# Performance work log

Measured on AMD Instinct MI355X. Metric: run time of the kernel, lower is better.

## Reference

```python
import jax, jax.numpy as jnp
from jax import lax
import numpy as np


def setup_inputs() -> dict:
    B, P, L, H, T = 4, 160, 128, 768, 9
    rng = np.random.default_rng(0)
    sent_length = rng.integers(L // 2, L + 1, size=B)
    sent_length[0] = L  # ensure max length equals L (pad_packed total_length)
    p2w = np.zeros((B, L, P), dtype=bool)
    for bi in range(B):
        pos = 1  # skip [CLS]
        for w in range(int(sent_length[bi])):
            n = 1 + int(rng.random() < 0.2)  # avg ~1.2 pieces per word
            if pos >= P - 1:
                break
            end = min(pos + n, P - 1)
            p2w[bi, w, pos:end] = True
            pos = end
    masks = np.arange(L)[None, :] < sent_length[:, None]
    labels = rng.integers(0, T, size=(B, L))
    key = jax.random.key(0)
    k1, k2, k3, k4, k5 = jax.random.split(key, 5)
    return {
        "bert_embs": jax.random.normal(k1, (B, P, H), jnp.float32),
        "pieces2word": jnp.asarray(p2w),
        "masks": jnp.asarray(masks),
        "labels": jnp.asarray(labels, jnp.int32),
        "sent_length": jnp.asarray(sent_length, jnp.int32),
        "W": jax.random.normal(k2, (H, T), jnp.float32) * 0.02,
        "b": jnp.zeros((T,), jnp.float32),
        "start_transitions": jax.random.uniform(k3, (T,), jnp.float32, -0.1, 0.1),
        "end_transitions": jax.random.uniform(k4, (T,), jnp.float32, -0.1, 0.1),
        "transitions": jax.random.uniform(k5, (T, T), jnp.float32, -0.1, 0.1),
    }


def crf_log_likelihood(emissions, tags, mask, start_t, end_t, trans):
    # torchcrf CRF forward (batch_first): log p(tags | emissions)
    B, L, T = emissions.shape
    maskf = mask.astype(emissions.dtype)
    barange = jnp.arange(B)
    # numerator: score of the gold tag sequence
    first_tags = tags[:, 0]
    num0 = start_t[first_tags] + emissions[barange, 0, first_tags]

    def num_step(s, inp):
        em_t, tp, tc, m = inp  # em_t: (B,T)
        return s + (trans[tp, tc] + em_t[barange, tc]) * m, None

    num, _ = lax.scan(
        num_step, num0,
        (emissions[:, 1:].transpose(1, 0, 2), tags[:, :-1].T, tags[:, 1:].T, maskf[:, 1:].T),
    )
    last_idx = jnp.sum(mask.astype(jnp.int32), axis=1) - 1
    num = num + end_t[tags[barange, last_idx]]
    # denominator: forward algorithm (log partition)
    alpha0 = start_t[None, :] + emissions[:, 0]  # (B,T)

    def den_step(a, inp):
        em_t, m = inp
        nxt = jax.nn.logsumexp(a[:, :, None] + trans[None, :, :] + em_t[:, None, :], axis=1)
        return jnp.where(m[:, None], nxt, a), None

    alpha, _ = lax.scan(den_step, alpha0, (emissions[:, 1:].transpose(1, 0, 2), mask[:, 1:].T))
    den = jax.nn.logsumexp(alpha + end_t[None, :], axis=1)
    return num - den


def reference(bert_embs, pieces2word, masks, labels, sent_length, W, b,
              start_transitions, end_transitions, transitions):
    min_value = lax.stop_gradient(jnp.min(bert_embs))  # .item() in torch detaches
    # expand + masked_fill + max over pieces: (B, L, P, H) -> (B, L, H)
    expanded = jnp.where(pieces2word[:, :, :, None], bert_embs[:, None, :, :], min_value)
    word_reps = jnp.max(expanded, axis=2)
    # pack_padded/pad_packed zeroes positions beyond sent_length
    word_reps = word_reps * masks[:, :, None].astype(word_reps.dtype)
    logits = word_reps @ W + b  # (B, L, T)
    llh = crf_log_likelihood(logits, labels, masks, start_transitions, end_transitions, transitions)
    loss = -jnp.sum(llh)  # module returns -1 * crf(...) (reduction='sum')
    return (loss, logits)
```

## Files before the change

### kernel.cpp

```cpp
#include <hip/hip_runtime.h>

#define NB 4
#define NP 160
#define NL 128
#define NH 768
#define NT 9
#define NBLK (NB * NL)
#define L2E 1.4426950408889634f
#define LN2 0.6931471805599453f

struct WS {
    float lg[NBLK * NT];
    float part[NBLK];
    int   empty[NBLK];
};

__device__ __forceinline__ float rdlane(float v, int p) {
    return __int_as_float(__builtin_amdgcn_readlane(__float_as_int(v), p));
}

__device__ __forceinline__ float dpp_add(float x) {
    float t;
#define STEP(ctrl, rmask, bc) \
    t = __int_as_float(__builtin_amdgcn_update_dpp(0, __float_as_int(x), ctrl, rmask, 0xf, bc)); \
    x += t;
    STEP(0x111, 0xf, true)
    STEP(0x112, 0xf, true)
    STEP(0x114, 0xf, true)
    STEP(0x118, 0xf, true)
    STEP(0x142, 0xa, false)
    STEP(0x143, 0xc, false)
#undef STEP
    return x;
}

__device__ __forceinline__ float dpp_fmin(float x) {
    float t;
#define STEP(ctrl, rmask) \
    t = __int_as_float(__builtin_amdgcn_update_dpp(__float_as_int(x), __float_as_int(x), ctrl, rmask, 0xf, false)); \
    x = fminf(x, t);
    STEP(0x111, 0xf) STEP(0x112, 0xf) STEP(0x114, 0xf) STEP(0x118, 0xf)
    STEP(0x142, 0xa) STEP(0x143, 0xc)
#undef STEP
    return x;
}

__global__ __launch_bounds__(256) void klogits(
    const float* __restrict__ embs, const void* __restrict__ p2w,
    const void* __restrict__ masks, const float* __restrict__ W,
    const float* __restrict__ bias, float* __restrict__ out_logits, WS* __restrict__ ws)
{
    const int bl = blockIdx.x;
    const int b  = bl / NL;
    const int tid = threadIdx.x;

    __shared__ float wrsh[NH];
    __shared__ int   plist[NP];
    __shared__ int   cnt;
    __shared__ int   isint_sh;
    __shared__ float wmin[4];

    const int base = bl * 960;
    float m = fminf(fminf(embs[base + tid], embs[base + tid + 256]), embs[base + tid + 512]);
    if (tid < 192) m = fminf(m, embs[base + tid + 768]);

    unsigned char pb = 0;
    if (tid < NP) pb = ((const unsigned char*)p2w)[bl * NP + tid];
    const unsigned char mkb = ((const unsigned char*)masks)[bl];

    if (tid == 0) { isint_sh = (((const unsigned*)masks)[0] <= 1u); cnt = 0; }
    __syncthreads();
    const int is_int = isint_sh;

    int have = 0;
    if (tid < NP) have = is_int ? (((const int*)p2w)[bl * NP + tid] != 0) : (pb != 0);
    if (have) plist[atomicAdd(&cnt, 1)] = tid;

    m = dpp_fmin(m);
    if ((tid & 63) == 63) wmin[tid >> 6] = m;

    const int mk = is_int ? (((const int*)masks)[bl] != 0) : (mkb != 0);
    __syncthreads();
    if (tid == 0) ws->part[bl] = fminf(fminf(wmin[0], wmin[1]), fminf(wmin[2], wmin[3]));

    const int nc = cnt;
    if (nc == 0) {
        if (tid == 0) ws->empty[bl] = mk ? 1 : 0;
        if (tid < NT) { float v = bias[tid]; out_logits[bl * NT + tid] = v; ws->lg[bl * NT + tid] = v; }
        return;
    }
    if (tid == 0) ws->empty[bl] = 0;

    #pragma unroll
    for (int k = 0; k < 3; k++) {
        int h = tid + k * 256;
        float wr = -3.0e38f;
        for (int i = 0; i < nc; i++)
            wr = fmaxf(wr, embs[(b * NP + plist[i]) * NH + h]);
        wrsh[h] = mk ? wr : 0.f;
    }
    __syncthreads();

    const int w = tid >> 6, lane = tid & 63;
    for (int t = w; t < NT; t += 4) {
        float acc = 0.f;
        #pragma unroll
        for (int j = 0; j < 12; j++) acc += wrsh[lane + j * 64] * W[(lane + j * 64) * NT + t];
        acc = dpp_add(acc);
        if (lane == 63) {
            float v = acc + bias[t];
            out_logits[bl * NT + t] = v;
            ws->lg[bl * NT + t]     = v;
        }
    }
}

__global__ __launch_bounds__(256) void kcrf(
    const int* __restrict__ labels, const int* __restrict__ sentlen,
    const float* __restrict__ W, const float* __restrict__ bias,
    const float* __restrict__ start_t, const float* __restrict__ end_t,
    const float* __restrict__ trans, WS* __restrict__ ws, float* __restrict__ out)
{
    __shared__ float em_s[NB * NL * NT + 16];
    __shared__ float trs[NT * NT];
    __shared__ int   lab_s[NB * NL];
    __shared__ float llh[NB];
    __shared__ float colsum[NT];
    __shared__ float wmin[4];

    const int tid  = threadIdx.x;
    const int w    = tid >> 6;
    const int lane = tid & 63;

    {
        const float4* s4 = (const float4*)ws->lg;
        float4* d4 = (float4*)em_s;
        #pragma unroll
        for (int i = tid; i < (NB * NL * NT) / 4; i += 256) d4[i] = s4[i];
        if (tid < (NB * NL) / 4) ((int4*)lab_s)[tid] = ((const int4*)labels)[tid];
        if (tid < NT * NT) trs[tid] = trans[tid] * L2E;
    }
    {
        float mv = fminf(ws->part[tid], ws->part[tid + 256]);
        mv = dpp_fmin(mv);
        if (lane == 63) wmin[w] = mv;
    }
    for (int t = w; t < NT; t += 4) {
        float s = 0.f;
        #pragma unroll
        for (int j = 0; j < 12; j++) s += W[(lane + j * 64) * NT + t];
        s = dpp_add(s);
        if (lane == 63) colsum[t] = s;
    }
    __syncthreads();
    const float minv = fminf(fminf(wmin[0], wmin[1]), fminf(wmin[2], wmin[3]));

    for (int r = tid; r < NBLK; r += 256) {
        if (ws->empty[r]) {
            #pragma unroll
            for (int t = 0; t < NT; t++) {
                float v = fmaf(minv, colsum[t], bias[t]);
                em_s[r * NT + t]   = v;
                out[1 + r * NT + t] = v;
            }
        }
    }
    __syncthreads();

    const int b   = w;
    const int c   = (lane < NT) ? lane : 0;
    const int len = sentlen[b];
    const float* em  = em_s + b * NL * NT;
    const int*   lab = lab_s + b * NL;

    float nsum = 0.f;
    for (int i = 1 + lane; i < len; i += 64) {
        int tp = lab[i - 1], tc = lab[i];
        nsum = fmaf(em[i * NT + tc], L2E, nsum + trs[tp * NT + tc]);
    }
    nsum = dpp_add(nsum);
    const float nsum_all = rdlane(nsum, 63);

    float tcol[NT];
    #pragma unroll
    for (int p = 0; p < NT; p++) tcol[p] = trs[p * NT + c];

    float a    = fmaf(em[c], L2E, start_t[c] * L2E);
    float em_c = em[NT + c];
    for (int i = 1; i < len; i++) {
        float em_nx = em[(i + 1) * NT + c];
        float v0 = rdlane(a, 0) + tcol[0];
        float e[8];
        #pragma unroll
        for (int p = 1; p < NT; p++) {
            float d = (rdlane(a, p) + tcol[p]) - v0;
            asm("v_exp_f32 %0, %1" : "=v"(e[p - 1]) : "v"(d));
        }
        float s = 1.0f + (((e[0] + e[1]) + (e[2] + e[3])) + ((e[4] + e[5]) + (e[6] + e[7])));
        float lg;
        asm("v_log_f32 %0, %1" : "=v"(lg) : "v"(s));
        a = fmaf(em_c, L2E, v0 + lg);
        em_c = em_nx;
    }

    float xv = a + end_t[c] * L2E;
    if (lane == 0) {
        float dv[NT];
        #pragma unroll
        for (int p = 0; p < NT; p++) dv[p] = rdlane(xv, p);
        float mx = fmaxf(fmaxf(fmaxf(dv[0], dv[1]), dv[2]),
                         fmaxf(fmaxf(fmaxf(dv[3], dv[4]), dv[5]),
                               fmaxf(fmaxf(dv[6], dv[7]), dv[8])));
        float s = 0.f;
        #pragma unroll
        for (int p = 0; p < NT; p++) {
            float d = dv[p] - mx, ee;
            asm("v_exp_f32 %0, %1" : "=v"(ee) : "v"(d));
            s += ee;
        }
        float lg;
        asm("v_log_f32 %0, %1" : "=v"(lg) : "v"(s));
        float den = mx + lg;
        int   t0  = lab[0];
        float num = fmaf(em[t0], L2E, nsum_all + start_t[t0] * L2E + end_t[lab[len - 1]] * L2E);
        llh[b] = (num - den) * LN2;
    }
    __syncthreads();
    if (tid == 0) out[0] = -(llh[0] + llh[1] + llh[2] + llh[3]);
}

extern "C" void kernel_launch(void* const* d_in, const int* in_sizes, int n_in,
                              void* d_out, int out_size, void* d_ws, size_t ws_size,
                              hipStream_t stream) {
    const float* embs    = (const float*)d_in[0];
    const void*  p2w     = d_in[1];
    const void*  masks   = d_in[2];
    const int*   labels  = (const int*)d_in[3];
    const int*   sentlen = (const int*)d_in[4];
    const float* W       = (const float*)d_in[5];
    const float* bias    = (const float*)d_in[6];
    const float* start_t = (const float*)d_in[7];
    const float* end_t   = (const float*)d_in[8];
    const float* trans   = (const float*)d_in[9];

    float* out = (float*)d_out;
    WS*    ws  = (WS*)d_ws;

    klogits<<<NBLK, 256, 0, stream>>>(embs, p2w, masks, W, bias, out + 1, ws);
    kcrf<<<1, 256, 0, stream>>>(labels, sentlen, W, bias, start_t, end_t, trans, ws, out);
}
```

Before: 33.94 us.

## Fuse logits and CRF kernels with a last-block-done atomic counter

Merges the per-word logits kernel and the single-block CRF kernel into one launch. Each block publishes its results with relaxed agent-scope atomic stores and increments a global counter, and the last block to arrive runs the CRF forward pass. This removes the second kernel launch and the gap between the two kernels. It adds a memset of the counter before each launch, a larger shared-memory footprint in every block, and depends on relaxed-ordering visibility plus an explicit vmcnt wait. The embedding min-load is also switched to float4 loads.

```diff
diff --git a/kernel.cpp b/kernel.cpp
--- a/kernel.cpp
+++ b/kernel.cpp
@@ -1,4 +1,5 @@
 #include <hip/hip_runtime.h>
+#include <stddef.h>
 
 #define NB 4
 #define NP 160
@@ -10,10 +11,14 @@
 #define LN2 0.6931471805599453f
 
 struct WS {
-    float lg[NBLK * NT];
-    float part[NBLK];
-    int   empty[NBLK];
+    float    lg[NBLK * NT];
+    float    part[NBLK];
+    unsigned flags[NBLK];
+    unsigned counter;
 };
+
+#define AST(p, v) __hip_atomic_store((p), (v), __ATOMIC_RELAXED, __HIP_MEMORY_SCOPE_AGENT)
+#define ALD(p)    __hip_atomic_load((p), __ATOMIC_RELAXED, __HIP_MEMORY_SCOPE_AGENT)
 
 __device__ __forceinline__ float rdlane(float v, int p) {
     return __int_as_float(__builtin_amdgcn_readlane(__float_as_int(v), p));
@@ -24,12 +29,8 @@
 #define STEP(ctrl, rmask, bc) \
     t = __int_as_float(__builtin_amdgcn_update_dpp(0, __float_as_int(x), ctrl, rmask, 0xf, bc)); \
     x += t;
-    STEP(0x111, 0xf, true)
-    STEP(0x112, 0xf, true)
-    STEP(0x114, 0xf, true)
-    STEP(0x118, 0xf, true)
-    STEP(0x142, 0xa, false)
-    STEP(0x143, 0xc, false)
+    STEP(0x111, 0xf, true) STEP(0x112, 0xf, true) STEP(0x114, 0xf, true) STEP(0x118, 0xf, true)
+    STEP(0x142, 0xa, false) STEP(0x143, 0xc, false)
 #undef STEP
     return x;
 }
@@ -45,10 +46,13 @@
     return x;
 }
 
-__global__ __launch_bounds__(256) void klogits(
+__global__ __launch_bounds__(256) void kfused(
     const float* __restrict__ embs, const void* __restrict__ p2w,
-    const void* __restrict__ masks, const float* __restrict__ W,
-    const float* __restrict__ bias, float* __restrict__ out_logits, WS* __restrict__ ws)
+    const void* __restrict__ masks, const int* __restrict__ labels,
+    const int* __restrict__ sentlen, const float* __restrict__ W,
+    const float* __restrict__ bias, const float* __restrict__ start_t,
+    const float* __restrict__ end_t, const float* __restrict__ trans,
+    float* __restrict__ out, WS* __restrict__ ws)
 {
     const int bl = blockIdx.x;
     const int b  = bl / NL;
@@ -59,11 +63,10 @@
     __shared__ int   cnt;
     __shared__ int   isint_sh;
     __shared__ float wmin[4];
-
-    const int base = bl * 960;
-    float m = fminf(fminf(embs[base + tid], embs[base + tid + 256]), embs[base + tid + 512]);
-    if (tid < 192) m = fminf(m, embs[base + tid + 768]);
-
+    __shared__ int   amlast;
+
+    const float4* e4 = (const float4*)(embs + bl * 960);
+    float4 mv4 = (tid < 240) ? e4[tid] : make_float4(3.0e38f, 3.0e38f, 3.0e38f, 3.0e38f);
     unsigned char pb = 0;
     if (tid < NP) pb = ((const unsigned char*)p2w)[bl * NP + tid];
     const unsigned char mkb = ((const unsigned char*)masks)[bl];
@@ -76,74 +79,69 @@
     if (tid < NP) have = is_int ? (((const int*)p2w)[bl * NP + tid] != 0) : (pb != 0);
     if (have) plist[atomicAdd(&cnt, 1)] = tid;
 
+    float m = fminf(fminf(mv4.x, mv4.y), fminf(mv4.z, mv4.w));
     m = dpp_fmin(m);
     if ((tid & 63) == 63) wmin[tid >> 6] = m;
 
     const int mk = is_int ? (((const int*)masks)[bl] != 0) : (mkb != 0);
     __syncthreads();
-    if (tid == 0) ws->part[bl] = fminf(fminf(wmin[0], wmin[1]), fminf(wmin[2], wmin[3]));
+    if (tid == 0) {
+        float pm = fminf(fminf(wmin[0], wmin[1]), fminf(wmin[2], wmin[3]));
+        AST(&ws->part[bl], pm);
+    }
 
     const int nc = cnt;
     if (nc == 0) {
-        if (tid == 0) ws->empty[bl] = mk ? 1 : 0;
-        if (tid < NT) { float v = bias[tid]; out_logits[bl * NT + tid] = v; ws->lg[bl * NT + tid] = v; }
-        return;
-    }
-    if (tid == 0) ws->empty[bl] = 0;
-
-    #pragma unroll
-    for (int k = 0; k < 3; k++) {
-        int h = tid + k * 256;
-        float wr = -3.0e38f;
-        for (int i = 0; i < nc; i++)
-            wr = fmaxf(wr, embs[(b * NP + plist[i]) * NH + h]);
-        wrsh[h] = mk ? wr : 0.f;
-    }
-    __syncthreads();
-
-    const int w = tid >> 6, lane = tid & 63;
-    for (int t = w; t < NT; t += 4) {
-        float acc = 0.f;
-        #pragma unroll
-        for (int j = 0; j < 12; j++) acc += wrsh[lane + j * 64] * W[(lane + j * 64) * NT + t];
-        acc = dpp_add(acc);
-        if (lane == 63) {
-            float v = acc + bias[t];
-            out_logits[bl * NT + t] = v;
-            ws->lg[bl * NT + t]     = v;
-        }
-    }
-}
-
-__global__ __launch_bounds__(256) void kcrf(
-    const int* __restrict__ labels, const int* __restrict__ sentlen,
-    const float* __restrict__ W, const float* __restrict__ bias,
-    const float* __restrict__ start_t, const float* __restrict__ end_t,
-    const float* __restrict__ trans, WS* __restrict__ ws, float* __restrict__ out)
-{
+        if (tid == 0) AST(&ws->flags[bl], mk ? 2u : 1u);
+    } else {
+        if (tid == 0) AST(&ws->flags[bl], 0u);
+        #pragma unroll
+        for (int k = 0; k < 3; k++) {
+            int h = tid + k * 256;
+            float wr = -3.0e38f;
+            for (int i = 0; i < nc; i++)
+                wr = fmaxf(wr, embs[(b * NP + plist[i]) * NH + h]);
+            wrsh[h] = mk ? wr : 0.f;
+        }
+        __syncthreads();
+        const int w = tid >> 6, lane = tid & 63;
+        for (int t = w; t < NT; t += 4) {
+            float acc = 0.f;
+            #pragma unroll
+            for (int j = 0; j < 12; j++) acc += wrsh[lane + j * 64] * W[(lane + j * 64) * NT + t];
+            acc = dpp_add(acc);
+            if (lane == 63) {
+                float v = acc + bias[t];
+                out[1 + bl * NT + t] = v;
+                AST(&ws->lg[bl * NT + t], v);
+            }
+        }
+    }
+
+    asm volatile("s_waitcnt vmcnt(0)" ::: "memory");
+    __syncthreads();
+    if (tid == 0) {
+        unsigned old = __hip_atomic_fetch_add(&ws->counter, 1u, __ATOMIC_RELAXED,
+                                              __HIP_MEMORY_SCOPE_AGENT);
+        amlast = (old == NBLK - 1);
+    }
+    __syncthreads();
+    if (!amlast) return;
+
     __shared__ float em_s[NB * NL * NT + 16];
     __shared__ float trs[NT * NT];
     __shared__ int   lab_s[NB * NL];
     __shared__ float llh[NB];
     __shared__ float colsum[NT];
-    __shared__ float wmin[4];
-
-    const int tid  = threadIdx.x;
+    __shared__ float wmin2[4];
+
     const int w    = tid >> 6;
     const int lane = tid & 63;
 
     {
-        const float4* s4 = (const float4*)ws->lg;
-        float4* d4 = (float4*)em_s;
-        #pragma unroll
-        for (int i = tid; i < (NB * NL * NT) / 4; i += 256) d4[i] = s4[i];
-        if (tid < (NB * NL) / 4) ((int4*)lab_s)[tid] = ((const int4*)labels)[tid];
-        if (tid < NT * NT) trs[tid] = trans[tid] * L2E;
-    }
-    {
-        float mv = fminf(ws->part[tid], ws->part[tid + 256]);
+        float mv = fminf(ALD(&ws->part[tid]), ALD(&ws->part[tid + 256]));
         mv = dpp_fmin(mv);
-        if (lane == 63) wmin[w] = mv;
+        if (lane == 63) wmin2[w] = mv;
     }
     for (int t = w; t < NT; t += 4) {
         float s = 0.f;
@@ -152,26 +150,38 @@
         s = dpp_add(s);
         if (lane == 63) colsum[t] = s;
     }
-    __syncthreads();
-    const float minv = fminf(fminf(wmin[0], wmin[1]), fminf(wmin[2], wmin[3]));
+    {
+        const unsigned long long* lg8 = (const unsigned long long*)ws->lg;
+        for (int i = tid; i < (NBLK * NT) / 2; i += 256) {
+            unsigned long long v = ALD(&lg8[i]);
+            em_s[2 * i]     = __int_as_float((unsigned)v);
+            em_s[2 * i + 1] = __int_as_float((unsigned)(v >> 32));
+        }
+    }
+    if (tid < (NB * NL) / 4) ((int4*)lab_s)[tid] = ((const int4*)labels)[tid];
+    if (tid < NT * NT) trs[tid] = trans[tid] * L2E;
+    __syncthreads();
+
+    const float minv = fminf(fminf(wmin2[0], wmin2[1]), fminf(wmin2[2], wmin2[3]));
 
     for (int r = tid; r < NBLK; r += 256) {
-        if (ws->empty[r]) {
+        unsigned f = ALD(&ws->flags[r]);
+        if (f) {
             #pragma unroll
             for (int t = 0; t < NT; t++) {
-                float v = fmaf(minv, colsum[t], bias[t]);
-                em_s[r * NT + t]   = v;
+                float v = (f == 2u) ? fmaf(minv, colsum[t], bias[t]) : bias[t];
+                em_s[r * NT + t]    = v;
                 out[1 + r * NT + t] = v;
             }
         }
     }
     __syncthreads();
 
-    const int b   = w;
+    const int bb  = w;
     const int c   = (lane < NT) ? lane : 0;
-    const int len = sentlen[b];
-    const float* em  = em_s + b * NL * NT;
-    const int*   lab = lab_s + b * NL;
+    const int len = sentlen[bb];
+    const float* em  = em_s + bb * NL * NT;
+    const int*   lab = lab_s + bb * NL;
 
     float nsum = 0.f;
     for (int i = 1 + lane; i < len; i += 64) {
@@ -223,7 +233,7 @@
         float den = mx + lg;
         int   t0  = lab[0];
         float num = fmaf(em[t0], L2E, nsum_all + start_t[t0] * L2E + end_t[lab[len - 1]] * L2E);
-        llh[b] = (num - den) * LN2;
+        llh[bb] = (num - den) * LN2;
     }
     __syncthreads();
     if (tid == 0) out[0] = -(llh[0] + llh[1] + llh[2] + llh[3]);
@@ -246,6 +256,7 @@
     float* out = (float*)d_out;
     WS*    ws  = (WS*)d_ws;
 
-    klogits<<<NBLK, 256, 0, stream>>>(embs, p2w, masks, W, bias, out + 1, ws);
-    kcrf<<<1, 256, 0, stream>>>(labels, sentlen, W, bias, start_t, end_t, trans, ws, out);
-}
+    hipMemsetAsync((char*)d_ws + offsetof(WS, counter), 0, sizeof(unsigned), stream);
+    kfused<<<NBLK, 256, 0, stream>>>(embs, p2w, masks, labels, sentlen, W, bias,
+                                     start_t, end_t, trans, out, ws);
+}
```

After: 45.19 us. 33.1% more time.

## Run CRF forward recursion in linear space with exponent rescaling; contiguous piece range

Applied to the files above, without the earlier changes.

The CRF forward algorithm moves from log space to linear probability space. Emissions are pre-exponentiated relative to tag 0 into shared memory, and transitions are exponentiated once. Each serial step becomes a 9x9 matrix-vector product with power-of-two renormalisation via ldexp, which removes eight exp and one log from the critical loop. In klogits, the atomic piece list is replaced by a ballot-based first/last range scan that assumes each word's pieces are contiguous. The kcrf global loads are also batched up front. The risks are numerical differences in the scaled linear recursion and the reliance on contiguous pieces.

```diff
diff --git a/kernel.cpp b/kernel.cpp
--- a/kernel.cpp
+++ b/kernel.cpp
@@ -24,12 +24,8 @@
 #define STEP(ctrl, rmask, bc) \
     t = __int_as_float(__builtin_amdgcn_update_dpp(0, __float_as_int(x), ctrl, rmask, 0xf, bc)); \
     x += t;
-    STEP(0x111, 0xf, true)
-    STEP(0x112, 0xf, true)
-    STEP(0x114, 0xf, true)
-    STEP(0x118, 0xf, true)
-    STEP(0x142, 0xa, false)
-    STEP(0x143, 0xc, false)
+    STEP(0x111, 0xf, true) STEP(0x112, 0xf, true) STEP(0x114, 0xf, true) STEP(0x118, 0xf, true)
+    STEP(0x142, 0xa, false) STEP(0x143, 0xc, false)
 #undef STEP
     return x;
 }
@@ -45,6 +41,10 @@
     return x;
 }
 
+__device__ __forceinline__ float exp2v(float x) {
+    float r; asm("v_exp_f32 %0, %1" : "=v"(r) : "v"(x)); return r;
+}
+
 __global__ __launch_bounds__(256) void klogits(
     const float* __restrict__ embs, const void* __restrict__ p2w,
     const void* __restrict__ masks, const float* __restrict__ W,
@@ -53,38 +53,45 @@
     const int bl = blockIdx.x;
     const int b  = bl / NL;
     const int tid = threadIdx.x;
+    const int w = tid >> 6, lane = tid & 63;
 
     __shared__ float wrsh[NH];
-    __shared__ int   plist[NP];
-    __shared__ int   cnt;
     __shared__ int   isint_sh;
     __shared__ float wmin[4];
-
-    const int base = bl * 960;
-    float m = fminf(fminf(embs[base + tid], embs[base + tid + 256]), embs[base + tid + 512]);
-    if (tid < 192) m = fminf(m, embs[base + tid + 768]);
-
+    __shared__ unsigned long long balsh[4];
+
+    const float4* e4 = (const float4*)(embs + bl * 960);
+    float4 mv4 = (tid < 240) ? e4[tid] : make_float4(3.0e38f, 3.0e38f, 3.0e38f, 3.0e38f);
     unsigned char pb = 0;
     if (tid < NP) pb = ((const unsigned char*)p2w)[bl * NP + tid];
     const unsigned char mkb = ((const unsigned char*)masks)[bl];
 
-    if (tid == 0) { isint_sh = (((const unsigned*)masks)[0] <= 1u); cnt = 0; }
+    if (tid == 0) isint_sh = (((const unsigned*)masks)[0] <= 1u);
     __syncthreads();
     const int is_int = isint_sh;
 
     int have = 0;
     if (tid < NP) have = is_int ? (((const int*)p2w)[bl * NP + tid] != 0) : (pb != 0);
-    if (have) plist[atomicAdd(&cnt, 1)] = tid;
-
+    unsigned long long bal = __ballot(have != 0);
+    if (lane == 0) balsh[w] = bal;
+
+    float m = fminf(fminf(mv4.x, mv4.y), fminf(mv4.z, mv4.w));
     m = dpp_fmin(m);
-    if ((tid & 63) == 63) wmin[tid >> 6] = m;
+    if (lane == 63) wmin[w] = m;
 
     const int mk = is_int ? (((const int*)masks)[bl] != 0) : (mkb != 0);
     __syncthreads();
     if (tid == 0) ws->part[bl] = fminf(fminf(wmin[0], wmin[1]), fminf(wmin[2], wmin[3]));
 
-    const int nc = cnt;
-    if (nc == 0) {
+    unsigned long long b0 = balsh[0], b1 = balsh[1], b2 = balsh[2];
+    int first = b0 ? (__ffsll((long long)b0) - 1)
+              : b1 ? (63 + __ffsll((long long)b1))
+              : b2 ? (127 + __ffsll((long long)b2)) : -1;
+    int last  = b2 ? (191 - __clzll((long long)b2))
+              : b1 ? (127 - __clzll((long long)b1))
+              : b0 ? (63 - __clzll((long long)b0)) : -1;
+
+    if (first < 0) {
         if (tid == 0) ws->empty[bl] = mk ? 1 : 0;
         if (tid < NT) { float v = bias[tid]; out_logits[bl * NT + tid] = v; ws->lg[bl * NT + tid] = v; }
         return;
@@ -95,13 +102,12 @@
     for (int k = 0; k < 3; k++) {
         int h = tid + k * 256;
         float wr = -3.0e38f;
-        for (int i = 0; i < nc; i++)
-            wr = fmaxf(wr, embs[(b * NP + plist[i]) * NH + h]);
+        for (int r = first; r <= last; r++)
+            wr = fmaxf(wr, embs[(b * NP + r) * NH + h]);
         wrsh[h] = mk ? wr : 0.f;
     }
     __syncthreads();
 
-    const int w = tid >> 6, lane = tid & 63;
     for (int t = w; t < NT; t += 4) {
         float acc = 0.f;
         #pragma unroll
@@ -122,6 +128,7 @@
     const float* __restrict__ trans, WS* __restrict__ ws, float* __restrict__ out)
 {
     __shared__ float em_s[NB * NL * NT + 16];
+    __shared__ float p_s[NB * NL * NT + 16];
     __shared__ float trs[NT * NT];
     __shared__ int   lab_s[NB * NL];
     __shared__ float llh[NB];
@@ -132,17 +139,24 @@
     const int w    = tid >> 6;
     const int lane = tid & 63;
 
+    const float4* s4 = (const float4*)ws->lg;
+    float4 lgv[4];
+    #pragma unroll
+    for (int r = 0; r < 4; r++) lgv[r] = s4[tid + r * 256];
+    float4 lgt = (tid < 128) ? s4[tid + 1024] : make_float4(0, 0, 0, 0);
+    int4  labv = (tid < 128) ? ((const int4*)labels)[tid] : make_int4(0, 0, 0, 0);
+    float pmv  = fminf(ws->part[tid], ws->part[tid + 256]);
+    float trv  = (tid < NT * NT) ? trans[tid] : 0.f;
+
+    float4* d4 = (float4*)em_s;
+    #pragma unroll
+    for (int r = 0; r < 4; r++) d4[tid + r * 256] = lgv[r];
+    if (tid < 128) d4[tid + 1024] = lgt;
+    if (tid < 128) ((int4*)lab_s)[tid] = labv;
+    if (tid < NT * NT) trs[tid] = trv * L2E;
+
     {
-        const float4* s4 = (const float4*)ws->lg;
-        float4* d4 = (float4*)em_s;
-        #pragma unroll
-        for (int i = tid; i < (NB * NL * NT) / 4; i += 256) d4[i] = s4[i];
-        if (tid < (NB * NL) / 4) ((int4*)lab_s)[tid] = ((const int4*)labels)[tid];
-        if (tid < NT * NT) trs[tid] = trans[tid] * L2E;
-    }
-    {
-        float mv = fminf(ws->part[tid], ws->part[tid + 256]);
-        mv = dpp_fmin(mv);
+        float mv = dpp_fmin(pmv);
         if (lane == 63) wmin[w] = mv;
     }
     for (int t = w; t < NT; t += 4) {
@@ -160,69 +174,78 @@
             #pragma unroll
             for (int t = 0; t < NT; t++) {
                 float v = fmaf(minv, colsum[t], bias[t]);
-                em_s[r * NT + t]   = v;
+                em_s[r * NT + t]    = v;
                 out[1 + r * NT + t] = v;
             }
         }
     }
     __syncthreads();
+
+    for (int j = tid; j < NB * NL * NT; j += 256) {
+        float em0 = em_s[(j / 9) * 9];
+        p_s[j] = exp2v((em_s[j] - em0) * L2E);
+    }
 
     const int b   = w;
     const int c   = (lane < NT) ? lane : 0;
     const int len = sentlen[b];
     const float* em  = em_s + b * NL * NT;
+    const float* ps  = p_s + b * NL * NT;
     const int*   lab = lab_s + b * NL;
 
-    float nsum = 0.f;
+    float nsum = 0.f, ksum = 0.f;
     for (int i = 1 + lane; i < len; i += 64) {
         int tp = lab[i - 1], tc = lab[i];
         nsum = fmaf(em[i * NT + tc], L2E, nsum + trs[tp * NT + tc]);
+        ksum = fmaf(em[i * NT], L2E, ksum);
     }
     nsum = dpp_add(nsum);
+    ksum = dpp_add(ksum);
     const float nsum_all = rdlane(nsum, 63);
-
-    float tcol[NT];
-    #pragma unroll
-    for (int p = 0; p < NT; p++) tcol[p] = trs[p * NT + c];
-
-    float a    = fmaf(em[c], L2E, start_t[c] * L2E);
-    float em_c = em[NT + c];
+    const float ksum_all = rdlane(ksum, 63);
+    __syncthreads();
+
+    float ecol[NT];
+    #pragma unroll
+    for (int p = 0; p < NT; p++) ecol[p] = exp2v(trs[p * NT + c]);
+
+    float a0  = (start_t[c] + em[c]) * L2E;
+    float a00 = rdlane(a0, 0);
+    float A   = exp2v(a0 - a00);
+    float Kf  = a00 + ksum_all;
+    int   Kl  = 0;
+
+    float p_nx = ps[NT + c];
     for (int i = 1; i < len; i++) {
-        float em_nx = em[(i + 1) * NT + c];
-        float v0 = rdlane(a, 0) + tcol[0];
-        float e[8];
+        float p_cur = p_nx;
+        p_nx = ps[(i + 1) * NT + c];
+        float r0 = rdlane(A, 0), r1 = rdlane(A, 1), r2 = rdlane(A, 2);
+        float r3 = rdlane(A, 3), r4 = rdlane(A, 4), r5 = rdlane(A, 5);
+        float r6 = rdlane(A, 6), r7 = rdlane(A, 7), r8 = rdlane(A, 8);
+        float s0 = r0 * ecol[0]; s0 = fmaf(r3, ecol[3], s0); s0 = fmaf(r6, ecol[6], s0);
+        float s1 = r1 * ecol[1]; s1 = fmaf(r4, ecol[4], s1); s1 = fmaf(r7, ecol[7], s1);
+        float s2 = r2 * ecol[2]; s2 = fmaf(r5, ecol[5], s2); s2 = fmaf(r8, ecol[8], s2);
+        float S  = (s0 + s1) + s2;
+        float mm = fmaxf(fmaxf(fmaxf(r0, r1), fmaxf(r2, r3)),
+                         fmaxf(fmaxf(r4, r5), fmaxf(r6, r7)));
+        mm = fmaxf(mm, r8);
+        int k = (__float_as_int(mm) >> 23) - 127;
+        float SP = S * p_cur;
+        int nk = -k;
+        asm("v_ldexp_f32 %0, %1, %2" : "=v"(A) : "v"(SP), "v"(nk));
+        Kl += k;
+    }
+
+    float xv = A * exp2v(end_t[c] * L2E);
+    if (lane == 0) {
+        float s = xv;
         #pragma unroll
-        for (int p = 1; p < NT; p++) {
-            float d = (rdlane(a, p) + tcol[p]) - v0;
-            asm("v_exp_f32 %0, %1" : "=v"(e[p - 1]) : "v"(d));
-        }
-        float s = 1.0f + (((e[0] + e[1]) + (e[2] + e[3])) + ((e[4] + e[5]) + (e[6] + e[7])));
+        for (int p = 1; p < NT; p++) s += rdlane(xv, p);
         float lg;
         asm("v_log_f32 %0, %1" : "=v"(lg) : "v"(s));
-        a = fmaf(em_c, L2E, v0 + lg);
-        em_c = em_nx;
-    }
-
-    float xv = a + end_t[c] * L2E;
-    if (lane == 0) {
-        float dv[NT];
-        #pragma unroll
-        for (int p = 0; p < NT; p++) dv[p] = rdlane(xv, p);
-        float mx = fmaxf(fmaxf(fmaxf(dv[0], dv[1]), dv[2]),
-                         fmaxf(fmaxf(fmaxf(dv[3], dv[4]), dv[5]),
-                               fmaxf(fmaxf(dv[6], dv[7]), dv[8])));
-        float s = 0.f;
-        #pragma unroll
-        for (int p = 0; p < NT; p++) {
-            float d = dv[p] - mx, ee;
-            asm("v_exp_f32 %0, %1" : "=v"(ee) : "v"(d));
-            s += ee;
-        }
-        float lg;
-        asm("v_log_f32 %0, %1" : "=v"(lg) : "v"(s));
-        float den = mx + lg;
+        float den = lg + Kf + (float)Kl;
         int   t0  = lab[0];
-        float num = fmaf(em[t0], L2E, nsum_all + start_t[t0] * L2E + end_t[lab[len - 1]] * L2E);
+        float num = nsum_all + (start_t[t0] + em[t0]) * L2E + end_t[lab[len - 1]] * L2E;
         llh[b] = (num - den) * LN2;
     }
     __syncthreads();
```

After: 29.36 us. -13.5%, faster.
